# Kernel tuning notes

Measured on AMD Instinct MI355X. Metric: run time of the kernel, lower is better.

Reference implementation:

```python
import jax, jax.numpy as jnp
import numpy as np

IC, HC, L, T, BS = 512, 512, 2, 512, 64
FORGET_BIAS = 1.0


def setup_inputs() -> dict:
    key = jax.random.key(0)
    k_x, k0, k1 = jax.random.split(key, 3)
    # xavier_normal std = sqrt(2/(fan_in+fan_out)), bias zeros (per module init)
    std0 = float(np.sqrt(2.0 / ((IC + HC) + 4 * HC)))
    std1 = float(np.sqrt(2.0 / ((HC + HC) + 4 * HC)))
    return {
        "x": jax.random.normal(k_x, (T, BS, IC), dtype=jnp.float32),
        "W0": jax.random.normal(k0, (IC + HC, 4 * HC), dtype=jnp.float32) * std0,
        "b0": jnp.zeros((4 * HC,), dtype=jnp.float32),
        "W1": jax.random.normal(k1, (HC + HC, 4 * HC), dtype=jnp.float32) * std1,
        "b1": jnp.zeros((4 * HC,), dtype=jnp.float32),
        "h0": jnp.zeros((L, 1, HC), dtype=jnp.float32),
        "c0": jnp.zeros((L, 1, HC), dtype=jnp.float32),
    }


def _run_layer(W, b, x_seq, h_init, c_init):
    def step(carry, xt):
        h, c = carry
        z = jnp.concatenate([xt, h], axis=1) @ W + b  # [bs, 4*hc]
        f, i, o, g = jnp.split(z, 4, axis=1)
        f = jax.nn.sigmoid(f + FORGET_BIAS)
        i = jax.nn.sigmoid(i)
        o = jax.nn.sigmoid(o)
        g = jnp.tanh(g)
        c = c * f + g * i
        h = o * jnp.tanh(c)
        return (h, c), h

    (hT, cT), hs = jax.lax.scan(step, (h_init, c_init), x_seq)
    return hs, hT, cT


def reference(x, W0, b0, W1, b1, h0, c0):
    bs = x.shape[1]
    h = jnp.broadcast_to(h0, (L, bs, HC))
    c = jnp.broadcast_to(c0, (L, bs, HC))
    params = [(W0, b0), (W1, b1)]
    lstm_input = x
    hs_final, cs_final = [], []
    for layer in range(L):
        W, b = params[layer]
        lstm_input, hT, cT = _run_layer(W, b, lstm_input, h[layer], c[layer])
        hs_final.append(hT)
        cs_final.append(cT)
    out = lstm_input  # [T, bs, hc]
    hs = jnp.stack(hs_final, axis=0)  # [L, bs, hc]
    cs = jnp.stack(cs_final, axis=0)
    return (out, (hs, cs))
```

## Files before the change

### kernel.cpp

```cpp
#include <hip/hip_runtime.h>
#include <cstdint>
#include <cstddef>


#define T_STEPS 512
#define WROW 1032
#define CAN64 0x7FC07FC07FC07FC0ULL

typedef float f32x4 __attribute__((ext_vector_type(4)));
typedef short s16x8 __attribute__((ext_vector_type(8)));

__device__ __forceinline__ unsigned short f2bf(float f) {
    unsigned int u = __builtin_bit_cast(unsigned int, f);
    u += 0x7FFFu + ((u >> 16) & 1u);
    return (unsigned short)(u >> 16);
}
__device__ __forceinline__ float sig_(float x)  { return 1.0f / (1.0f + __expf(-x)); }
__device__ __forceinline__ float tanh_(float x) { return 1.0f - 2.0f / (__expf(2.0f * x) + 1.0f); }

__device__ __forceinline__ unsigned long long ld8(const unsigned short* p) {
    return __hip_atomic_load((unsigned long long*)p, __ATOMIC_RELAXED, __HIP_MEMORY_SCOPE_AGENT);
}
__device__ __forceinline__ void stc(unsigned short* p, s16x8 v) {
    ulonglong2 u = __builtin_bit_cast(ulonglong2, v);
    __hip_atomic_store((unsigned long long*)p,     u.x, __ATOMIC_RELAXED, __HIP_MEMORY_SCOPE_AGENT);
    __hip_atomic_store((unsigned long long*)p + 1, u.y, __ATOMIC_RELAXED, __HIP_MEMORY_SCOPE_AGENT);
}


__global__ void k_conv_bf16(const float* __restrict__ src, unsigned short* __restrict__ dst) {
    int i = (blockIdx.x * 256 + threadIdx.x) * 8;
    float4 a = *(const float4*)(src + i);
    float4 b = *(const float4*)(src + i + 4);
    s16x8 o;
    o[0]=(short)f2bf(a.x); o[1]=(short)f2bf(a.y); o[2]=(short)f2bf(a.z); o[3]=(short)f2bf(a.w);
    o[4]=(short)f2bf(b.x); o[5]=(short)f2bf(b.y); o[6]=(short)f2bf(b.z); o[7]=(short)f2bf(b.w);
    *(s16x8*)(dst + i) = o;
}

__global__ void k_transpose_w(const float* __restrict__ W0, const float* __restrict__ W1,
                              unsigned short* __restrict__ WT0, unsigned short* __restrict__ WT1) {
    __shared__ unsigned short tile[32][33];
    const float* W = blockIdx.z ? W1 : W0;
    unsigned short* WT = blockIdx.z ? WT1 : WT0;
    int n0 = blockIdx.x * 32, k0 = blockIdx.y * 32;
    int tx = threadIdx.x, ty = threadIdx.y;
    #pragma unroll
    for (int i = 0; i < 4; i++)
        tile[ty + i*8][tx] = f2bf(W[(size_t)(k0 + ty + i*8) * 2048 + n0 + tx]);
    __syncthreads();
    #pragma unroll
    for (int i = 0; i < 4; i++)
        WT[(size_t)(n0 + ty + i*8) * 1024 + k0 + tx] = tile[tx][ty + i*8];
}

__global__ void k_hinit(const float* __restrict__ h0, unsigned short* __restrict__ hi0,
                        unsigned short* __restrict__ hi1) {
    int idx = blockIdx.x * 256 + threadIdx.x;
    int layer = idx >> 15;
    int r = idx & 32767;
    int b = r >> 9;
    int j = r & 511;
    unsigned short v = f2bf(h0[layer * 512 + j]);
    unsigned short* d = layer ? hi1 : hi0;
    d[(size_t)((j >> 3) * 64 + b) * 8 + (j & 7)] = v;
}

__global__ void k_fill_canary(unsigned long long* __restrict__ dst) {
    size_t i = ((size_t)blockIdx.x * 256 + threadIdx.x) * 2;
    dst[i]     = CAN64;
    dst[i + 1] = CAN64;
}

__global__ __launch_bounds__(256, 1) void k_lstm_fused5(
    const unsigned short* __restrict__ xb,
    const unsigned short* __restrict__ hi0, const unsigned short* __restrict__ hi1,
    const unsigned short* __restrict__ WT0, const unsigned short* __restrict__ WT1,
    const float* __restrict__ b0, const float* __restrict__ b1,
    const float* __restrict__ c0,
    unsigned short* __restrict__ h0s, unsigned short* __restrict__ h1s,
    float* __restrict__ out, float* __restrict__ hs, float* __restrict__ cs)
{
    __shared__ unsigned short Wl[32][WROW];
    __shared__ unsigned short hst[64][8];

    const int isl1 = (int)(blockIdx.x >> 6);
    const int wg   = (int)(blockIdx.x & 63);
    const int tid  = (int)threadIdx.x;
    const int j0   = wg * 8;

    {
        const unsigned short* WT = isl1 ? WT1 : WT0;
        #pragma unroll
        for (int it = 0; it < 16; it++) {
            int idx = it * 256 + tid;
            int row = idx >> 7;
            int ch  = idx & 127;
            int gate = (row >> 4) * 2 + ((row & 15) >> 3);
            int gr = gate * 512 + j0 + (row & 7);
            *(s16x8*)(&Wl[row][ch * 8]) = *(const s16x8*)(WT + (size_t)gr * 1024 + ch * 8);
        }
    }
    __syncthreads();

    const int lane = tid & 63;
    const int wv   = tid >> 6;
    const int q    = lane >> 4;
    const int cc   = lane & 15;
    const int arow = wv * 16 + cc;
    const int jj   = j0 + (cc & 7);
    const int bb   = wv * 16 + q * 4;

    const float* bias = isl1 ? b1 : b0;
    const float bt0 = (cc < 8) ? bias[jj] : bias[512 + jj];
    const float bt1 = (cc < 8) ? bias[1024 + jj] : bias[1536 + jj];
    float cst[4];
    { float ci = c0[isl1 * 512 + jj]; cst[0]=cst[1]=cst[2]=cst[3]=ci; }

    if (!isl1) {
        for (int t = 0; t < T_STEPS; t++) {
            s16x8 ax[16];
            {
                const unsigned short* xp = xb + (size_t)(t * 64 + arow) * 512 + q * 8;
                #pragma unroll
                for (int kk = 0; kk < 16; kk++)
                    ax[kk] = *(const s16x8*)(xp + kk * 32);
            }

            s16x8 ah[16];
            const unsigned short* hb = t ? (h0s + (size_t)(t - 1) * 32768) : hi0;
            bool ok = true;
            #pragma unroll
            for (int kk = 0; kk < 16; kk++) {
                const unsigned short* p = hb + ((size_t)(kk * 4 + q) * 64 + arow) * 8;
                unsigned long long lo = ld8(p), hi = ld8(p + 4);
                ok = ok & (lo != CAN64) & (hi != CAN64);
                ulonglong2 u; u.x = lo; u.y = hi;
                ah[kk] = __builtin_bit_cast(s16x8, u);
            }

            f32x4 a0  = {bt0, bt0, bt0, bt0};
            f32x4 a1  = {bt1, bt1, bt1, bt1};
            f32x4 a0b = {0.f, 0.f, 0.f, 0.f};
            f32x4 a1b = {0.f, 0.f, 0.f, 0.f};
            #pragma unroll
            for (int kk = 0; kk < 16; kk += 2) {
                s16x8 w00 = *(const s16x8*)(&Wl[cc][kk * 32 + q * 8]);
                s16x8 w10 = *(const s16x8*)(&Wl[16 + cc][kk * 32 + q * 8]);
                a0  = __builtin_amdgcn_mfma_f32_16x16x32_bf16(ax[kk], w00, a0, 0, 0, 0);
                a1  = __builtin_amdgcn_mfma_f32_16x16x32_bf16(ax[kk], w10, a1, 0, 0, 0);
                s16x8 w01 = *(const s16x8*)(&Wl[cc][(kk + 1) * 32 + q * 8]);
                s16x8 w11 = *(const s16x8*)(&Wl[16 + cc][(kk + 1) * 32 + q * 8]);
                a0b = __builtin_amdgcn_mfma_f32_16x16x32_bf16(ax[kk + 1], w01, a0b, 0, 0, 0);
                a1b = __builtin_amdgcn_mfma_f32_16x16x32_bf16(ax[kk + 1], w11, a1b, 0, 0, 0);
            }

            while (!ok) {
                __builtin_amdgcn_s_sleep(1);
                ok = true;
                #pragma unroll
                for (int kk = 0; kk < 16; kk++) {
                    const unsigned short* p = hb + ((size_t)(kk * 4 + q) * 64 + arow) * 8;
                    unsigned long long lo = ld8(p), hi = ld8(p + 4);
                    ok = ok & (lo != CAN64) & (hi != CAN64);
                    ulonglong2 u; u.x = lo; u.y = hi;
                    ah[kk] = __builtin_bit_cast(s16x8, u);
                }
            }

            #pragma unroll
            for (int kk = 0; kk < 16; kk += 2) {
                s16x8 w00 = *(const s16x8*)(&Wl[cc][(16 + kk) * 32 + q * 8]);
                s16x8 w10 = *(const s16x8*)(&Wl[16 + cc][(16 + kk) * 32 + q * 8]);
                a0  = __builtin_amdgcn_mfma_f32_16x16x32_bf16(ah[kk], w00, a0, 0, 0, 0);
                a1  = __builtin_amdgcn_mfma_f32_16x16x32_bf16(ah[kk], w10, a1, 0, 0, 0);
                s16x8 w01 = *(const s16x8*)(&Wl[cc][(17 + kk) * 32 + q * 8]);
                s16x8 w11 = *(const s16x8*)(&Wl[16 + cc][(17 + kk) * 32 + q * 8]);
                a0b = __builtin_amdgcn_mfma_f32_16x16x32_bf16(ah[kk + 1], w01, a0b, 0, 0, 0);
                a1b = __builtin_amdgcn_mfma_f32_16x16x32_bf16(ah[kk + 1], w11, a1b, 0, 0, 0);
            }
            a0 = a0 + a0b;
            a1 = a1 + a1b;

            #pragma unroll
            for (int r = 0; r < 4; r++) {
                float z0 = a0[r], z1 = a1[r];
                float p0 = __shfl_xor(z0, 8, 64);
                float p1 = __shfl_xor(z1, 8, 64);
                float zf = (cc < 8) ? z0 : p0;
                float zi = (cc < 8) ? p0 : z0;
                float zo = (cc < 8) ? z1 : p1;
                float zg = (cc < 8) ? p1 : z1;
                float fg = sig_(zf + 1.0f);
                float ig = sig_(zi);
                float og = sig_(zo);
                float gg = tanh_(zg);
                float cn = cst[r] * fg + gg * ig;
                cst[r] = cn;
                float hv = og * tanh_(cn);
                int b = bb + r;
                if (cc < 8) hst[b][cc] = f2bf(hv);
                if (t == T_STEPS - 1) {
                    if (cc < 8) hs[(size_t)b * 512 + jj] = hv;
                    else        cs[(size_t)b * 512 + jj] = cn;
                }
            }

            if (lane < 16) {
                int row = wv * 16 + lane;
                stc(h0s + (size_t)t * 32768 + (size_t)wg * 512 + (size_t)row * 8,
                    *(const s16x8*)(&hst[row][0]));
            }
        }
    } else {
        for (int t = 0; t < T_STEPS; t++) {
            s16x8 ah1[16];
            const unsigned short* hb1 = t ? (h1s + (size_t)(t - 1) * 32768) : hi1;
            bool ok1 = true;
            #pragma unroll
            for (int kk = 0; kk < 16; kk++) {
                const unsigned short* p = hb1 + ((size_t)(kk * 4 + q) * 64 + arow) * 8;
                unsigned long long lo = ld8(p), hi = ld8(p + 4);
                ok1 = ok1 & (lo != CAN64) & (hi != CAN64);
                ulonglong2 u; u.x = lo; u.y = hi;
                ah1[kk] = __builtin_bit_cast(s16x8, u);
            }
            while (!ok1) {
                __builtin_amdgcn_s_sleep(1);
                ok1 = true;
                #pragma unroll
                for (int kk = 0; kk < 16; kk++) {
                    const unsigned short* p = hb1 + ((size_t)(kk * 4 + q) * 64 + arow) * 8;
                    unsigned long long lo = ld8(p), hi = ld8(p + 4);
                    ok1 = ok1 & (lo != CAN64) & (hi != CAN64);
                    ulonglong2 u; u.x = lo; u.y = hi;
                    ah1[kk] = __builtin_bit_cast(s16x8, u);
                }
            }

            s16x8 ah0[16];
            const unsigned short* hb0 = h0s + (size_t)t * 32768;
            bool ok0 = true;
            #pragma unroll
            for (int kk = 0; kk < 16; kk++) {
                const unsigned short* p = hb0 + ((size_t)(kk * 4 + q) * 64 + arow) * 8;
                unsigned long long lo = ld8(p), hi = ld8(p + 4);
                ok0 = ok0 & (lo != CAN64) & (hi != CAN64);
                ulonglong2 u; u.x = lo; u.y = hi;
                ah0[kk] = __builtin_bit_cast(s16x8, u);
            }

            f32x4 a0  = {bt0, bt0, bt0, bt0};
            f32x4 a1  = {bt1, bt1, bt1, bt1};
            f32x4 a0b = {0.f, 0.f, 0.f, 0.f};
            f32x4 a1b = {0.f, 0.f, 0.f, 0.f};
            #pragma unroll
            for (int kk = 0; kk < 16; kk += 2) {
                s16x8 w00 = *(const s16x8*)(&Wl[cc][(16 + kk) * 32 + q * 8]);
                s16x8 w10 = *(const s16x8*)(&Wl[16 + cc][(16 + kk) * 32 + q * 8]);
                a0  = __builtin_amdgcn_mfma_f32_16x16x32_bf16(ah1[kk], w00, a0, 0, 0, 0);
                a1  = __builtin_amdgcn_mfma_f32_16x16x32_bf16(ah1[kk], w10, a1, 0, 0, 0);
                s16x8 w01 = *(const s16x8*)(&Wl[cc][(17 + kk) * 32 + q * 8]);
                s16x8 w11 = *(const s16x8*)(&Wl[16 + cc][(17 + kk) * 32 + q * 8]);
                a0b = __builtin_amdgcn_mfma_f32_16x16x32_bf16(ah1[kk + 1], w01, a0b, 0, 0, 0);
                a1b = __builtin_amdgcn_mfma_f32_16x16x32_bf16(ah1[kk + 1], w11, a1b, 0, 0, 0);
            }

            while (!ok0) {
                __builtin_amdgcn_s_sleep(1);
                ok0 = true;
                #pragma unroll
                for (int kk = 0; kk < 16; kk++) {
                    const unsigned short* p = hb0 + ((size_t)(kk * 4 + q) * 64 + arow) * 8;
                    unsigned long long lo = ld8(p), hi = ld8(p + 4);
                    ok0 = ok0 & (lo != CAN64) & (hi != CAN64);
                    ulonglong2 u; u.x = lo; u.y = hi;
                    ah0[kk] = __builtin_bit_cast(s16x8, u);
                }
            }

            #pragma unroll
            for (int kk = 0; kk < 16; kk += 2) {
                s16x8 w00 = *(const s16x8*)(&Wl[cc][kk * 32 + q * 8]);
                s16x8 w10 = *(const s16x8*)(&Wl[16 + cc][kk * 32 + q * 8]);
                a0  = __builtin_amdgcn_mfma_f32_16x16x32_bf16(ah0[kk], w00, a0, 0, 0, 0);
                a1  = __builtin_amdgcn_mfma_f32_16x16x32_bf16(ah0[kk], w10, a1, 0, 0, 0);
                s16x8 w01 = *(const s16x8*)(&Wl[cc][(kk + 1) * 32 + q * 8]);
                s16x8 w11 = *(const s16x8*)(&Wl[16 + cc][(kk + 1) * 32 + q * 8]);
                a0b = __builtin_amdgcn_mfma_f32_16x16x32_bf16(ah0[kk + 1], w01, a0b, 0, 0, 0);
                a1b = __builtin_amdgcn_mfma_f32_16x16x32_bf16(ah0[kk + 1], w11, a1b, 0, 0, 0);
            }
            a0 = a0 + a0b;
            a1 = a1 + a1b;

            float ov[4];
            #pragma unroll
            for (int r = 0; r < 4; r++) {
                float z0 = a0[r], z1 = a1[r];
                float p0 = __shfl_xor(z0, 8, 64);
                float p1 = __shfl_xor(z1, 8, 64);
                float zf = (cc < 8) ? z0 : p0;
                float zi = (cc < 8) ? p0 : z0;
                float zo = (cc < 8) ? z1 : p1;
                float zg = (cc < 8) ? p1 : z1;
                float fg = sig_(zf + 1.0f);
                float ig = sig_(zi);
                float og = sig_(zo);
                float gg = tanh_(zg);
                float cn = cst[r] * fg + gg * ig;
                cst[r] = cn;
                float hv = og * tanh_(cn);
                ov[r] = hv;
                int b = bb + r;
                if (cc < 8) hst[b][cc] = f2bf(hv);
                if (t == T_STEPS - 1) {
                    if (cc < 8) hs[(size_t)(64 + b) * 512 + jj] = hv;
                    else        cs[(size_t)(64 + b) * 512 + jj] = cn;
                }
            }

            if (lane < 16) {
                int row = wv * 16 + lane;
                stc(h1s + (size_t)t * 32768 + (size_t)wg * 512 + (size_t)row * 8,
                    *(const s16x8*)(&hst[row][0]));
            }

            if (cc >= 8) {
                #pragma unroll
                for (int r = 0; r < 4; r++)
                    out[((size_t)(t * 64 + bb + r)) * 512 + jj] = ov[r];
            }
        }
    }
}


extern "C" void kernel_launch(void* const* d_in, const int* in_sizes, int n_in,
                              void* d_out, int out_size, void* d_ws, size_t ws_size,
                              hipStream_t stream) {
    const float* x  = (const float*)d_in[0];
    const float* W0 = (const float*)d_in[1];
    const float* b0 = (const float*)d_in[2];
    const float* W1 = (const float*)d_in[3];
    const float* b1 = (const float*)d_in[4];
    const float* h0 = (const float*)d_in[5];
    const float* c0 = (const float*)d_in[6];
    float* out = (float*)d_out;

    char* ws = (char*)d_ws;
    unsigned short* xb  = (unsigned short*)(ws);
    unsigned short* h0s = (unsigned short*)(ws + 33554432);
    unsigned short* h1s = (unsigned short*)(ws + 2 * 33554432);
    unsigned short* WT0 = (unsigned short*)(ws + 3 * 33554432);
    unsigned short* WT1 = (unsigned short*)(ws + 3 * 33554432 + 4194304);
    unsigned short* hi0 = (unsigned short*)(ws + 3 * 33554432 + 2 * 4194304);
    unsigned short* hi1 = (unsigned short*)(ws + 3 * 33554432 + 2 * 4194304 + 65536);

    k_fill_canary<<<16384, 256, 0, stream>>>((unsigned long long*)h0s);
    k_conv_bf16<<<8192, 256, 0, stream>>>(x, xb);
    k_transpose_w<<<dim3(64, 32, 2), dim3(32, 8), 0, stream>>>(W0, W1, WT0, WT1);
    k_hinit<<<256, 256, 0, stream>>>(h0, hi0, hi1);

    float* hs = out + 16777216;
    float* cs = hs + 65536;
    k_lstm_fused5<<<128, 256, 0, stream>>>(xb, hi0, hi1, WT0, WT1, b0, b1, c0,
                                           h0s, h1s, out, hs, cs);
}
```

Baseline: 2.810 ms.

## Shrink LSTM workgroups to one wave looping over four batch chunks

The persistent LSTM kernel now launches 64-thread workgroups instead of 256. Each single wave loops serially over the four 16-row batch chunks that four waves used to handle in parallel. The cell state becomes a 4x4 register array and the shared staging buffer shrinks to 16 rows. This cuts intra-block parallelism per step by four, in exchange for a simpler per-chunk pipeline and less contention. Each chunk's h is published as soon as it is ready, so downstream consumers can start earlier, but the serial chain per timestep gets longer.

Result: slower. 5.907 ms (+110.2%).

```diff
diff --git a/kernel.cpp b/kernel.cpp
--- a/kernel.cpp
+++ b/kernel.cpp
@@ -72,7 +72,7 @@
     dst[i + 1] = CAN64;
 }
 
-__global__ __launch_bounds__(256, 1) void k_lstm_fused5(
+__global__ __launch_bounds__(64, 1) void k_lstm_fused10(
     const unsigned short* __restrict__ xb,
     const unsigned short* __restrict__ hi0, const unsigned short* __restrict__ hi1,
     const unsigned short* __restrict__ WT0, const unsigned short* __restrict__ WT1,
@@ -82,7 +82,7 @@
     float* __restrict__ out, float* __restrict__ hs, float* __restrict__ cs)
 {
     __shared__ unsigned short Wl[32][WROW];
-    __shared__ unsigned short hst[64][8];
+    __shared__ unsigned short hst[16][8];
 
     const int isl1 = (int)(blockIdx.x >> 6);
     const int wg   = (int)(blockIdx.x & 63);
@@ -92,8 +92,8 @@
     {
         const unsigned short* WT = isl1 ? WT1 : WT0;
         #pragma unroll
-        for (int it = 0; it < 16; it++) {
-            int idx = it * 256 + tid;
+        for (int it = 0; it < 64; it++) {
+            int idx = it * 64 + tid;
             int row = idx >> 7;
             int ch  = idx & 127;
             int gate = (row >> 4) * 2 + ((row & 15) >> 3);
@@ -103,232 +103,240 @@
     }
     __syncthreads();
 
-    const int lane = tid & 63;
-    const int wv   = tid >> 6;
-    const int q    = lane >> 4;
-    const int cc   = lane & 15;
-    const int arow = wv * 16 + cc;
-    const int jj   = j0 + (cc & 7);
-    const int bb   = wv * 16 + q * 4;
+    const int q  = tid >> 4;
+    const int cc = tid & 15;
+    const int jj = j0 + (cc & 7);
 
     const float* bias = isl1 ? b1 : b0;
     const float bt0 = (cc < 8) ? bias[jj] : bias[512 + jj];
     const float bt1 = (cc < 8) ? bias[1024 + jj] : bias[1536 + jj];
-    float cst[4];
-    { float ci = c0[isl1 * 512 + jj]; cst[0]=cst[1]=cst[2]=cst[3]=ci; }
+    float cst[4][4];
+    {
+        float ci = c0[isl1 * 512 + jj];
+        #pragma unroll
+        for (int c = 0; c < 4; c++)
+            #pragma unroll
+            for (int r = 0; r < 4; r++)
+                cst[c][r] = ci;
+    }
 
     if (!isl1) {
         for (int t = 0; t < T_STEPS; t++) {
-            s16x8 ax[16];
-            {
+            const unsigned short* hb = t ? (h0s + (size_t)(t - 1) * 32768) : hi0;
+            #pragma unroll
+            for (int c = 0; c < 4; c++) {
+                const int arow = c * 16 + cc;
+
+                s16x8 ah[16];
+                #pragma unroll
+                for (int kk = 0; kk < 16; kk++) {
+                    const unsigned short* p = hb + ((size_t)(kk * 4 + q) * 64 + arow) * 8;
+                    ulonglong2 u; u.x = ld8(p); u.y = ld8(p + 4);
+                    ah[kk] = __builtin_bit_cast(s16x8, u);
+                }
+
                 const unsigned short* xp = xb + (size_t)(t * 64 + arow) * 512 + q * 8;
-                #pragma unroll
-                for (int kk = 0; kk < 16; kk++)
-                    ax[kk] = *(const s16x8*)(xp + kk * 32);
-            }
-
-            s16x8 ah[16];
-            const unsigned short* hb = t ? (h0s + (size_t)(t - 1) * 32768) : hi0;
-            bool ok = true;
-            #pragma unroll
-            for (int kk = 0; kk < 16; kk++) {
-                const unsigned short* p = hb + ((size_t)(kk * 4 + q) * 64 + arow) * 8;
-                unsigned long long lo = ld8(p), hi = ld8(p + 4);
-                ok = ok & (lo != CAN64) & (hi != CAN64);
-                ulonglong2 u; u.x = lo; u.y = hi;
-                ah[kk] = __builtin_bit_cast(s16x8, u);
-            }
-
-            f32x4 a0  = {bt0, bt0, bt0, bt0};
-            f32x4 a1  = {bt1, bt1, bt1, bt1};
-            f32x4 a0b = {0.f, 0.f, 0.f, 0.f};
-            f32x4 a1b = {0.f, 0.f, 0.f, 0.f};
-            #pragma unroll
-            for (int kk = 0; kk < 16; kk += 2) {
-                s16x8 w00 = *(const s16x8*)(&Wl[cc][kk * 32 + q * 8]);
-                s16x8 w10 = *(const s16x8*)(&Wl[16 + cc][kk * 32 + q * 8]);
-                a0  = __builtin_amdgcn_mfma_f32_16x16x32_bf16(ax[kk], w00, a0, 0, 0, 0);
-                a1  = __builtin_amdgcn_mfma_f32_16x16x32_bf16(ax[kk], w10, a1, 0, 0, 0);
-                s16x8 w01 = *(const s16x8*)(&Wl[cc][(kk + 1) * 32 + q * 8]);
-                s16x8 w11 = *(const s16x8*)(&Wl[16 + cc][(kk + 1) * 32 + q * 8]);
-                a0b = __builtin_amdgcn_mfma_f32_16x16x32_bf16(ax[kk + 1], w01, a0b, 0, 0, 0);
-                a1b = __builtin_amdgcn_mfma_f32_16x16x32_bf16(ax[kk + 1], w11, a1b, 0, 0, 0);
-            }
-
-            while (!ok) {
-                __builtin_amdgcn_s_sleep(1);
-                ok = true;
-                #pragma unroll
-                for (int kk = 0; kk < 16; kk++) {
-                    const unsigned short* p = hb + ((size_t)(kk * 4 + q) * 64 + arow) * 8;
-                    unsigned long long lo = ld8(p), hi = ld8(p + 4);
-                    ok = ok & (lo != CAN64) & (hi != CAN64);
-                    ulonglong2 u; u.x = lo; u.y = hi;
-                    ah[kk] = __builtin_bit_cast(s16x8, u);
-                }
-            }
-
-            #pragma unroll
-            for (int kk = 0; kk < 16; kk += 2) {
-                s16x8 w00 = *(const s16x8*)(&Wl[cc][(16 + kk) * 32 + q * 8]);
-                s16x8 w10 = *(const s16x8*)(&Wl[16 + cc][(16 + kk) * 32 + q * 8]);
-                a0  = __builtin_amdgcn_mfma_f32_16x16x32_bf16(ah[kk], w00, a0, 0, 0, 0);
-                a1  = __builtin_amdgcn_mfma_f32_16x16x32_bf16(ah[kk], w10, a1, 0, 0, 0);
-                s16x8 w01 = *(const s16x8*)(&Wl[cc][(17 + kk) * 32 + q * 8]);
-                s16x8 w11 = *(const s16x8*)(&Wl[16 + cc][(17 + kk) * 32 + q * 8]);
-                a0b = __builtin_amdgcn_mfma_f32_16x16x32_bf16(ah[kk + 1], w01, a0b, 0, 0, 0);
-                a1b = __builtin_amdgcn_mfma_f32_16x16x32_bf16(ah[kk + 1], w11, a1b, 0, 0, 0);
-            }
-            a0 = a0 + a0b;
-            a1 = a1 + a1b;
-
-            #pragma unroll
-            for (int r = 0; r < 4; r++) {
-                float z0 = a0[r], z1 = a1[r];
-                float p0 = __shfl_xor(z0, 8, 64);
-                float p1 = __shfl_xor(z1, 8, 64);
-                float zf = (cc < 8) ? z0 : p0;
-                float zi = (cc < 8) ? p0 : z0;
-                float zo = (cc < 8) ? z1 : p1;
-                float zg = (cc < 8) ? p1 : z1;
-                float fg = sig_(zf + 1.0f);
-                float ig = sig_(zi);
-                float og = sig_(zo);
-                float gg = tanh_(zg);
-                float cn = cst[r] * fg + gg * ig;
-                cst[r] = cn;
-                float hv = og * tanh_(cn);
-                int b = bb + r;
-                if (cc < 8) hst[b][cc] = f2bf(hv);
-                if (t == T_STEPS - 1) {
-                    if (cc < 8) hs[(size_t)b * 512 + jj] = hv;
-                    else        cs[(size_t)b * 512 + jj] = cn;
-                }
-            }
-
-            if (lane < 16) {
-                int row = wv * 16 + lane;
-                stc(h0s + (size_t)t * 32768 + (size_t)wg * 512 + (size_t)row * 8,
-                    *(const s16x8*)(&hst[row][0]));
+                f32x4 a0  = {bt0, bt0, bt0, bt0};
+                f32x4 a1  = {bt1, bt1, bt1, bt1};
+                f32x4 a0b = {0.f, 0.f, 0.f, 0.f};
+                f32x4 a1b = {0.f, 0.f, 0.f, 0.f};
+                #pragma unroll
+                for (int kk = 0; kk < 16; kk += 2) {
+                    s16x8 x0 = *(const s16x8*)(xp + kk * 32);
+                    s16x8 x1 = *(const s16x8*)(xp + (kk + 1) * 32);
+                    s16x8 w00 = *(const s16x8*)(&Wl[cc][kk * 32 + q * 8]);
+                    s16x8 w10 = *(const s16x8*)(&Wl[16 + cc][kk * 32 + q * 8]);
+                    a0  = __builtin_amdgcn_mfma_f32_16x16x32_bf16(x0, w00, a0, 0, 0, 0);
+                    a1  = __builtin_amdgcn_mfma_f32_16x16x32_bf16(x0, w10, a1, 0, 0, 0);
+                    s16x8 w01 = *(const s16x8*)(&Wl[cc][(kk + 1) * 32 + q * 8]);
+                    s16x8 w11 = *(const s16x8*)(&Wl[16 + cc][(kk + 1) * 32 + q * 8]);
+                    a0b = __builtin_amdgcn_mfma_f32_16x16x32_bf16(x1, w01, a0b, 0, 0, 0);
+                    a1b = __builtin_amdgcn_mfma_f32_16x16x32_bf16(x1, w11, a1b, 0, 0, 0);
+                }
+
+                bool ok = true;
+                #pragma unroll
+                for (int kk = 0; kk < 16; kk++) {
+                    ulonglong2 u = __builtin_bit_cast(ulonglong2, ah[kk]);
+                    ok = ok & (u.x != CAN64) & (u.y != CAN64);
+                }
+                while (!ok) {
+                    __builtin_amdgcn_s_sleep(1);
+                    ok = true;
+                    #pragma unroll
+                    for (int kk = 0; kk < 16; kk++) {
+                        const unsigned short* p = hb + ((size_t)(kk * 4 + q) * 64 + arow) * 8;
+                        ulonglong2 u; u.x = ld8(p); u.y = ld8(p + 4);
+                        ok = ok & (u.x != CAN64) & (u.y != CAN64);
+                        ah[kk] = __builtin_bit_cast(s16x8, u);
+                    }
+                }
+
+                #pragma unroll
+                for (int kk = 0; kk < 16; kk += 2) {
+                    s16x8 w00 = *(const s16x8*)(&Wl[cc][(16 + kk) * 32 + q * 8]);
+                    s16x8 w10 = *(const s16x8*)(&Wl[16 + cc][(16 + kk) * 32 + q * 8]);
+                    a0  = __builtin_amdgcn_mfma_f32_16x16x32_bf16(ah[kk], w00, a0, 0, 0, 0);
+                    a1  = __builtin_amdgcn_mfma_f32_16x16x32_bf16(ah[kk], w10, a1, 0, 0, 0);
+                    s16x8 w01 = *(const s16x8*)(&Wl[cc][(17 + kk) * 32 + q * 8]);
+                    s16x8 w11 = *(const s16x8*)(&Wl[16 + cc][(17 + kk) * 32 + q * 8]);
+                    a0b = __builtin_amdgcn_mfma_f32_16x16x32_bf16(ah[kk + 1], w01, a0b, 0, 0, 0);
+                    a1b = __builtin_amdgcn_mfma_f32_16x16x32_bf16(ah[kk + 1], w11, a1b, 0, 0, 0);
+                }
+                a0 = a0 + a0b;
+                a1 = a1 + a1b;
+
+                #pragma unroll
+                for (int r = 0; r < 4; r++) {
+                    float z0 = a0[r], z1 = a1[r];
+                    float p0 = __shfl_xor(z0, 8, 64);
+                    float p1 = __shfl_xor(z1, 8, 64);
+                    float zf = (cc < 8) ? z0 : p0;
+                    float zi = (cc < 8) ? p0 : z0;
+                    float zo = (cc < 8) ? z1 : p1;
+                    float zg = (cc < 8) ? p1 : z1;
+                    float fg = sig_(zf + 1.0f);
+                    float ig = sig_(zi);
+                    float og = sig_(zo);
+                    float gg = tanh_(zg);
+                    float cn = cst[c][r] * fg + gg * ig;
+                    cst[c][r] = cn;
+                    float hv = og * tanh_(cn);
+                    if (cc < 8) hst[q * 4 + r][cc] = f2bf(hv);
+                    if (t == T_STEPS - 1) {
+                        int b = c * 16 + q * 4 + r;
+                        if (cc < 8) hs[(size_t)b * 512 + jj] = hv;
+                        else        cs[(size_t)b * 512 + jj] = cn;
+                    }
+                }
+                if (tid < 16)
+                    stc(h0s + (size_t)t * 32768 + (size_t)wg * 512 + (size_t)(c * 16 + tid) * 8,
+                        *(const s16x8*)(&hst[tid][0]));
             }
         }
     } else {
         for (int t = 0; t < T_STEPS; t++) {
-            s16x8 ah1[16];
             const unsigned short* hb1 = t ? (h1s + (size_t)(t - 1) * 32768) : hi1;
-            bool ok1 = true;
+            const unsigned short* hb0 = h0s + (size_t)t * 32768;
             #pragma unroll
-            for (int kk = 0; kk < 16; kk++) {
-                const unsigned short* p = hb1 + ((size_t)(kk * 4 + q) * 64 + arow) * 8;
-                unsigned long long lo = ld8(p), hi = ld8(p + 4);
-                ok1 = ok1 & (lo != CAN64) & (hi != CAN64);
-                ulonglong2 u; u.x = lo; u.y = hi;
-                ah1[kk] = __builtin_bit_cast(s16x8, u);
-            }
-            while (!ok1) {
-                __builtin_amdgcn_s_sleep(1);
-                ok1 = true;
+            for (int c = 0; c < 4; c++) {
+                const int arow = c * 16 + cc;
+
+                s16x8 ah1[16];
                 #pragma unroll
                 for (int kk = 0; kk < 16; kk++) {
                     const unsigned short* p = hb1 + ((size_t)(kk * 4 + q) * 64 + arow) * 8;
-                    unsigned long long lo = ld8(p), hi = ld8(p + 4);
-                    ok1 = ok1 & (lo != CAN64) & (hi != CAN64);
-                    ulonglong2 u; u.x = lo; u.y = hi;
+                    ulonglong2 u; u.x = ld8(p); u.y = ld8(p + 4);
                     ah1[kk] = __builtin_bit_cast(s16x8, u);
                 }
-            }
-
-            s16x8 ah0[16];
-            const unsigned short* hb0 = h0s + (size_t)t * 32768;
-            bool ok0 = true;
-            #pragma unroll
-            for (int kk = 0; kk < 16; kk++) {
-                const unsigned short* p = hb0 + ((size_t)(kk * 4 + q) * 64 + arow) * 8;
-                unsigned long long lo = ld8(p), hi = ld8(p + 4);
-                ok0 = ok0 & (lo != CAN64) & (hi != CAN64);
-                ulonglong2 u; u.x = lo; u.y = hi;
-                ah0[kk] = __builtin_bit_cast(s16x8, u);
-            }
-
-            f32x4 a0  = {bt0, bt0, bt0, bt0};
-            f32x4 a1  = {bt1, bt1, bt1, bt1};
-            f32x4 a0b = {0.f, 0.f, 0.f, 0.f};
-            f32x4 a1b = {0.f, 0.f, 0.f, 0.f};
-            #pragma unroll
-            for (int kk = 0; kk < 16; kk += 2) {
-                s16x8 w00 = *(const s16x8*)(&Wl[cc][(16 + kk) * 32 + q * 8]);
-                s16x8 w10 = *(const s16x8*)(&Wl[16 + cc][(16 + kk) * 32 + q * 8]);
-                a0  = __builtin_amdgcn_mfma_f32_16x16x32_bf16(ah1[kk], w00, a0, 0, 0, 0);
-                a1  = __builtin_amdgcn_mfma_f32_16x16x32_bf16(ah1[kk], w10, a1, 0, 0, 0);
-                s16x8 w01 = *(const s16x8*)(&Wl[cc][(17 + kk) * 32 + q * 8]);
-                s16x8 w11 = *(const s16x8*)(&Wl[16 + cc][(17 + kk) * 32 + q * 8]);
-                a0b = __builtin_amdgcn_mfma_f32_16x16x32_bf16(ah1[kk + 1], w01, a0b, 0, 0, 0);
-                a1b = __builtin_amdgcn_mfma_f32_16x16x32_bf16(ah1[kk + 1], w11, a1b, 0, 0, 0);
-            }
-
-            while (!ok0) {
-                __builtin_amdgcn_s_sleep(1);
-                ok0 = true;
+                s16x8 ah0[16];
                 #pragma unroll
                 for (int kk = 0; kk < 16; kk++) {
                     const unsigned short* p = hb0 + ((size_t)(kk * 4 + q) * 64 + arow) * 8;
-                    unsigned long long lo = ld8(p), hi = ld8(p + 4);
-                    ok0 = ok0 & (lo != CAN64) & (hi != CAN64);
-                    ulonglong2 u; u.x = lo; u.y = hi;
+                    ulonglong2 u; u.x = ld8(p); u.y = ld8(p + 4);
                     ah0[kk] = __builtin_bit_cast(s16x8, u);
                 }
-            }
-
-            #pragma unroll
-            for (int kk = 0; kk < 16; kk += 2) {
-                s16x8 w00 = *(const s16x8*)(&Wl[cc][kk * 32 + q * 8]);
-                s16x8 w10 = *(const s16x8*)(&Wl[16 + cc][kk * 32 + q * 8]);
-                a0  = __builtin_amdgcn_mfma_f32_16x16x32_bf16(ah0[kk], w00, a0, 0, 0, 0);
-                a1  = __builtin_amdgcn_mfma_f32_16x16x32_bf16(ah0[kk], w10, a1, 0, 0, 0);
-                s16x8 w01 = *(const s16x8*)(&Wl[cc][(kk + 1) * 32 + q * 8]);
-                s16x8 w11 = *(const s16x8*)(&Wl[16 + cc][(kk + 1) * 32 + q * 8]);
-                a0b = __builtin_amdgcn_mfma_f32_16x16x32_bf16(ah0[kk + 1], w01, a0b, 0, 0, 0);
-                a1b = __builtin_amdgcn_mfma_f32_16x16x32_bf16(ah0[kk + 1], w11, a1b, 0, 0, 0);
-            }
-            a0 = a0 + a0b;
-            a1 = a1 + a1b;
-
-            float ov[4];
-            #pragma unroll
-            for (int r = 0; r < 4; r++) {
-                float z0 = a0[r], z1 = a1[r];
-                float p0 = __shfl_xor(z0, 8, 64);
-                float p1 = __shfl_xor(z1, 8, 64);
-                float zf = (cc < 8) ? z0 : p0;
-                float zi = (cc < 8) ? p0 : z0;
-                float zo = (cc < 8) ? z1 : p1;
-                float zg = (cc < 8) ? p1 : z1;
-                float fg = sig_(zf + 1.0f);
-                float ig = sig_(zi);
-                float og = sig_(zo);
-                float gg = tanh_(zg);
-                float cn = cst[r] * fg + gg * ig;
-                cst[r] = cn;
-                float hv = og * tanh_(cn);
-                ov[r] = hv;
-                int b = bb + r;
-                if (cc < 8) hst[b][cc] = f2bf(hv);
-                if (t == T_STEPS - 1) {
-                    if (cc < 8) hs[(size_t)(64 + b) * 512 + jj] = hv;
-                    else        cs[(size_t)(64 + b) * 512 + jj] = cn;
-                }
-            }
-
-            if (lane < 16) {
-                int row = wv * 16 + lane;
-                stc(h1s + (size_t)t * 32768 + (size_t)wg * 512 + (size_t)row * 8,
-                    *(const s16x8*)(&hst[row][0]));
-            }
-
-            if (cc >= 8) {
-                #pragma unroll
-                for (int r = 0; r < 4; r++)
-                    out[((size_t)(t * 64 + bb + r)) * 512 + jj] = ov[r];
+
+                bool ok1 = true;
+                #pragma unroll
+                for (int kk = 0; kk < 16; kk++) {
+                    ulonglong2 u = __builtin_bit_cast(ulonglong2, ah1[kk]);
+                    ok1 = ok1 & (u.x != CAN64) & (u.y != CAN64);
+                }
+                while (!ok1) {
+                    __builtin_amdgcn_s_sleep(1);
+                    ok1 = true;
+                    #pragma unroll
+                    for (int kk = 0; kk < 16; kk++) {
+                        const unsigned short* p = hb1 + ((size_t)(kk * 4 + q) * 64 + arow) * 8;
+                        ulonglong2 u; u.x = ld8(p); u.y = ld8(p + 4);
+                        ok1 = ok1 & (u.x != CAN64) & (u.y != CAN64);
+                        ah1[kk] = __builtin_bit_cast(s16x8, u);
+                    }
+                }
+
+                f32x4 a0  = {bt0, bt0, bt0, bt0};
+                f32x4 a1  = {bt1, bt1, bt1, bt1};
+                f32x4 a0b = {0.f, 0.f, 0.f, 0.f};
+                f32x4 a1b = {0.f, 0.f, 0.f, 0.f};
+                #pragma unroll
+                for (int kk = 0; kk < 16; kk += 2) {
+                    s16x8 w00 = *(const s16x8*)(&Wl[cc][(16 + kk) * 32 + q * 8]);
+                    s16x8 w10 = *(const s16x8*)(&Wl[16 + cc][(16 + kk) * 32 + q * 8]);
+                    a0  = __builtin_amdgcn_mfma_f32_16x16x32_bf16(ah1[kk], w00, a0, 0, 0, 0);
+                    a1  = __builtin_amdgcn_mfma_f32_16x16x32_bf16(ah1[kk], w10, a1, 0, 0, 0);
+                    s16x8 w01 = *(const s16x8*)(&Wl[cc][(17 + kk) * 32 + q * 8]);
+                    s16x8 w11 = *(const s16x8*)(&Wl[16 + cc][(17 + kk) * 32 + q * 8]);
+                    a0b = __builtin_amdgcn_mfma_f32_16x16x32_bf16(ah1[kk + 1], w01, a0b, 0, 0, 0);
+                    a1b = __builtin_amdgcn_mfma_f32_16x16x32_bf16(ah1[kk + 1], w11, a1b, 0, 0, 0);
+                }
+
+                bool ok0 = true;
+                #pragma unroll
+                for (int kk = 0; kk < 16; kk++) {
+                    ulonglong2 u = __builtin_bit_cast(ulonglong2, ah0[kk]);
+                    ok0 = ok0 & (u.x != CAN64) & (u.y != CAN64);
+                }
+                while (!ok0) {
+                    __builtin_amdgcn_s_sleep(1);
+                    ok0 = true;
+                    #pragma unroll
+                    for (int kk = 0; kk < 16; kk++) {
+                        const unsigned short* p = hb0 + ((size_t)(kk * 4 + q) * 64 + arow) * 8;
+                        ulonglong2 u; u.x = ld8(p); u.y = ld8(p + 4);
+                        ok0 = ok0 & (u.x != CAN64) & (u.y != CAN64);
+                        ah0[kk] = __builtin_bit_cast(s16x8, u);
+                    }
+                }
+
+                #pragma unroll
+                for (int kk = 0; kk < 16; kk += 2) {
+                    s16x8 w00 = *(const s16x8*)(&Wl[cc][kk * 32 + q * 8]);
+                    s16x8 w10 = *(const s16x8*)(&Wl[16 + cc][kk * 32 + q * 8]);
+                    a0  = __builtin_amdgcn_mfma_f32_16x16x32_bf16(ah0[kk], w00, a0, 0, 0, 0);
+                    a1  = __builtin_amdgcn_mfma_f32_16x16x32_bf16(ah0[kk], w10, a1, 0, 0, 0);
+                    s16x8 w01 = *(const s16x8*)(&Wl[cc][(kk + 1) * 32 + q * 8]);
+                    s16x8 w11 = *(const s16x8*)(&Wl[16 + cc][(kk + 1) * 32 + q * 8]);
+                    a0b = __builtin_amdgcn_mfma_f32_16x16x32_bf16(ah0[kk + 1], w01, a0b, 0, 0, 0);
+                    a1b = __builtin_amdgcn_mfma_f32_16x16x32_bf16(ah0[kk + 1], w11, a1b, 0, 0, 0);
+                }
+                a0 = a0 + a0b;
+                a1 = a1 + a1b;
+
+                float ov[4];
+                #pragma unroll
+                for (int r = 0; r < 4; r++) {
+                    float z0 = a0[r], z1 = a1[r];
+                    float p0 = __shfl_xor(z0, 8, 64);
+                    float p1 = __shfl_xor(z1, 8, 64);
+                    float zf = (cc < 8) ? z0 : p0;
+                    float zi = (cc < 8) ? p0 : z0;
+                    float zo = (cc < 8) ? z1 : p1;
+                    float zg = (cc < 8) ? p1 : z1;
+                    float fg = sig_(zf + 1.0f);
+                    float ig = sig_(zi);
+                    float og = sig_(zo);
+                    float gg = tanh_(zg);
+                    float cn = cst[c][r] * fg + gg * ig;
+                    cst[c][r] = cn;
+                    float hv = og * tanh_(cn);
+                    ov[r] = hv;
+                    if (cc < 8) hst[q * 4 + r][cc] = f2bf(hv);
+                    if (t == T_STEPS - 1) {
+                        int b = c * 16 + q * 4 + r;
+                        if (cc < 8) hs[(size_t)(64 + b) * 512 + jj] = hv;
+                        else        cs[(size_t)(64 + b) * 512 + jj] = cn;
+                    }
+                }
+                if (tid < 16)
+                    stc(h1s + (size_t)t * 32768 + (size_t)wg * 512 + (size_t)(c * 16 + tid) * 8,
+                        *(const s16x8*)(&hst[tid][0]));
+
+                if (cc >= 8) {
+                    #pragma unroll
+                    for (int r = 0; r < 4; r++)
+                        out[((size_t)(t * 64 + c * 16 + q * 4 + r)) * 512 + jj] = ov[r];
+                }
             }
         }
     }
@@ -363,6 +371,6 @@
 
     float* hs = out + 16777216;
     float* cs = hs + 65536;
-    k_lstm_fused5<<<128, 256, 0, stream>>>(xb, hi0, hi1, WT0, WT1, b0, b1, c0,
+    k_lstm_fused10<<<128, 64, 0, stream>>>(xb, hi0, hi1, WT0, WT1, b0, b1, c0,
                                            h0s, h1s, out, hs, cs);
 }
```
